# Optimization experiments

Measured on AMD Instinct MI355X. Metric: run time of the kernel, lower is better.

The kernel has to match this reference:

```python
import jax, jax.numpy as jnp
import numpy as np

B, C, H, W = 8, 3, 512, 512
EPS = 2e-4
N_ITER = 10  # n_iter_max default in TvChambolleDenoiser.forward


def setup_inputs() -> dict:
    key = jax.random.key(0)
    k1, k2 = jax.random.split(key)
    image = jax.random.normal(k1, (B, C, H, W), dtype=jnp.float32)
    # per-image denoising strength, typical TV weights
    weight = jax.random.uniform(k2, (B,), dtype=jnp.float32, minval=0.05, maxval=0.15)
    return {"image": image, "weight": weight}


def _denoise_tv_2d(img, w, eps=EPS, n_iter=N_ITER):
    """Chambolle TV denoising of a single 2D image (faithful to the torch loop)."""
    tau = 0.25  # 1 / (2 * ndim), ndim = 2
    numel = img.shape[0] * img.shape[1]

    def body(carry, i):
        pt, out, E_init, E_prev, done = carry
        # divergence of dual variable pt: dt = -pt.sum(0); dt[1:,:] += pt[0,:-1,:]; dt[:,1:] += pt[1,:,:-1]
        dt = -(pt[0] + pt[1])
        dt = dt.at[1:, :].add(pt[0, :-1, :])
        dt = dt.at[:, 1:].add(pt[1, :, :-1])
        out_new = jnp.where(i > 0, img + dt, img)
        Et = jnp.where(i > 0, jnp.sum(dt * dt), jnp.float32(0.0))
        # forward finite differences, zero-padded at the far boundary (gt stays 0 there)
        g0 = jnp.pad(out_new[1:, :] - out_new[:-1, :], ((0, 1), (0, 0)))
        g1 = jnp.pad(out_new[:, 1:] - out_new[:, :-1], ((0, 0), (0, 1)))
        s = g0 * g0 + g1 * g1
        # safe sqrt (forward value identical; avoids NaN grads at exact zeros)
        norm = jnp.sqrt(jnp.where(s > 0, s, 1.0)) * (s > 0)
        Et = (Et + w * jnp.sum(norm)) / numel
        gt = jnp.stack([g0, g1])  # [2, H, W]
        pt_new = (pt - tau * gt) / (1.0 + (tau / w) * norm)[None]
        E_init_new = jnp.where(i == 0, Et, E_init)
        converged = (i > 0) & (jnp.abs(E_prev - Et) < eps * E_init_new)
        # once converged (break in the torch loop), freeze all state
        pt = jnp.where(done, pt, pt_new)
        out = jnp.where(done, out, out_new)
        E_prev = jnp.where(done, E_prev, Et)
        E_init = jnp.where(done, E_init, E_init_new)
        done = done | converged
        return (pt, out, E_init, E_prev, done), None

    carry0 = (
        jnp.zeros((2,) + img.shape, img.dtype),  # pt
        img,                                      # out
        jnp.float32(0.0),                         # E_init
        jnp.float32(0.0),                         # E_previous
        jnp.bool_(False),                         # done
    )
    (pt, out, E_init, E_prev, done), _ = jax.lax.scan(body, carry0, jnp.arange(n_iter))
    return out


def reference(image, weight):
    b, c, h, w = image.shape
    imgs = image.reshape(b * c, h, w)          # each (batch, channel) slice denoised independently
    ws = jnp.repeat(weight, c)                 # per-batch weight shared across channels
    out = jax.vmap(_denoise_tv_2d)(imgs, ws)
    return out.reshape(b, c, h, w)
```

## Files before the change

### kernel.cpp

```cpp
#include <hip/hip_runtime.h>
#include <hip/hip_fp16.h>
#include <math.h>
#include <stdint.h>

#define HH 512
#define WW 512
#define NIMG 24
#define CCH 3
#define TAU 0.25f
#define TVEPS 2e-4f
#define NUMEL 262144.0f

#define LSF 69
#define LSH 70


__device__ __forceinline__ float2 h2f(uint32_t v) {
    __half2 h; *reinterpret_cast<uint32_t*>(&h) = v;
    return __half22float2(h);
}
__device__ __forceinline__ uint32_t f2h2(float a, float b) {
    __half2 h = __floats2half2_rn(a, b);
    return *reinterpret_cast<uint32_t*>(&h);
}
__device__ __forceinline__ void h4_to_f(uint2 hv, float* f) {
    float2 a = h2f(hv.x), b = h2f(hv.y);
    f[0] = a.x; f[1] = a.y; f[2] = b.x; f[3] = b.y;
}

struct Smem {
    uint32_t PT[68 * LSF];
    float    OA[68 * LSF];
    __half   IM[68 * LSH];
};

__device__ __forceinline__ int SUMIX(int slot, int arr, int im) {
    return ((slot * 4 + arr) * NIMG + im) * 64;
}

__device__ void stage_pt_im(Smem& S, const uint32_t* __restrict__ ptg,
                            const __half* __restrict__ hI,
                            int x0, int y0, int tid) {
    for (int idx = tid; idx < 68 * 34; idx += 256) {
        int r = idx / 34, mq = idx - r * 34;
        int c = 2 * mq;
        int y = y0 - 2 + r, x = x0 - 2 + c;
        uint2 pv = make_uint2(0u, 0u);
        uint32_t iv = 0u;
        if ((unsigned)y < (unsigned)HH && (unsigned)x < (unsigned)WW) {
            size_t off = (size_t)y * WW + x;
            pv = *(const uint2*)(ptg + off);
            iv = *(const uint32_t*)(hI + off);
        }
        S.PT[r * LSF + c] = pv.x;
        S.PT[r * LSF + c + 1] = pv.y;
        *(uint32_t*)&S.IM[r * LSH + c] = iv;
    }
}

template <bool ACC>
__device__ float phase_outA(Smem& S, int tid) {
    float acc = 0.f;
    for (int idx = tid; idx < 67 * 67; idx += 256) {
        int r = idx / 67, c = idx - r * 67;
        r += 1; c += 1;
        float2 cf = h2f(S.PT[r * LSF + c]);
        float up = h2f(S.PT[(r - 1) * LSF + c]).x;
        float lf = h2f(S.PT[r * LSF + c - 1]).y;
        float im = __half2float(S.IM[r * LSH + c]);
        float oa = im + (-(cf.x + cf.y) + up + lf);
        S.OA[r * LSF + c] = oa;
        if (ACC) {
            if (r >= 2 && r < 66 && c >= 2 && c < 66) {
                float d = oa - im;
                acc += d * d;
            }
        }
    }
    return acc;
}

template <bool ACC>
__device__ float phase_ptA(Smem& S, int x0, int y0, int tid, float tw) {
    float acc = 0.f;
    for (int idx = tid; idx < 66 * 66; idx += 256) {
        int r = idx / 66, c = idx - r * 66;
        r += 1; c += 1;
        int y = y0 - 2 + r, x = x0 - 2 + c;
        if ((unsigned)y < (unsigned)HH && (unsigned)x < (unsigned)WW) {
            float o = S.OA[r * LSF + c];
            float g0 = (y < HH - 1) ? S.OA[(r + 1) * LSF + c] - o : 0.f;
            float g1 = (x < WW - 1) ? S.OA[r * LSF + c + 1] - o : 0.f;
            float ss2 = g0 * g0 + g1 * g1;
            float nrm = (ss2 > 0.f) ? sqrtf(ss2) : 0.f;
            if (ACC) {
                if (r >= 2 && r < 66 && c >= 2 && c < 66) acc += nrm;
            }
            float inv = __builtin_amdgcn_rcpf(1.f + tw * nrm);
            float2 cf = h2f(S.PT[r * LSF + c]);
            S.PT[r * LSF + c] = f2h2((cf.x - TAU * g0) * inv, (cf.y - TAU * g1) * inv);
        } else {
            S.PT[r * LSF + c] = 0u;
        }
    }
    return acc;
}

template <bool ACC>
__device__ float phase_outB(Smem& S, int tid) {
    float acc = 0.f;
    for (int idx = tid; idx < 65 * 65; idx += 256) {
        int r = idx / 65, c = idx - r * 65;
        r += 2; c += 2;
        float2 cf = h2f(S.PT[r * LSF + c]);
        float im = __half2float(S.IM[r * LSH + c]);
        float ob = im + (-(cf.x + cf.y) + h2f(S.PT[(r - 1) * LSF + c]).x
                         + h2f(S.PT[r * LSF + c - 1]).y);
        S.OA[r * LSF + c] = ob;
        if (ACC) {
            if (r < 66 && c < 66) {
                float d = ob - im;
                acc += d * d;
            }
        }
    }
    return acc;
}

__device__ float phase_ptB_store(Smem& S, uint32_t* __restrict__ poutI,
                                 int x0, int y0, int tid, float tw) {
    const int tx = tid & 15, ry = tid >> 4;
    const int gxb = x0 + 4 * tx;
    float acc = 0.f;
    #pragma unroll
    for (int i = 0; i < 4; ++i) {
        int gy = y0 + ry + 16 * i;
        int r = 2 + ry + 16 * i;
        uint32_t pv[4];
        #pragma unroll
        for (int j = 0; j < 4; ++j) {
            int c = 2 + 4 * tx + j;
            float o = S.OA[r * LSF + c];
            float g0 = (gy < HH - 1) ? S.OA[(r + 1) * LSF + c] - o : 0.f;
            float g1 = (gxb + j < WW - 1) ? S.OA[r * LSF + c + 1] - o : 0.f;
            float ss2 = g0 * g0 + g1 * g1;
            float nrm = (ss2 > 0.f) ? sqrtf(ss2) : 0.f;
            acc += nrm;
            float inv = __builtin_amdgcn_rcpf(1.f + tw * nrm);
            float2 cf = h2f(S.PT[r * LSF + c]);
            pv[j] = f2h2((cf.x - TAU * g0) * inv, (cf.y - TAU * g1) * inv);
        }
        *(uint4*)(poutI + (size_t)gy * WW + gxb) = make_uint4(pv[0], pv[1], pv[2], pv[3]);
    }
    return acc;
}

__device__ __forceinline__ void red4_store(float a, float b, float c, float d,
                                           float* pa, float* pb, float* pc, float* pdd,
                                           int tid) {
    for (int off = 32; off > 0; off >>= 1) {
        a += __shfl_down(a, off, 64);
        b += __shfl_down(b, off, 64);
        c += __shfl_down(c, off, 64);
        d += __shfl_down(d, off, 64);
    }
    __shared__ float sr[4][4];
    int wave = tid >> 6, lane = tid & 63;
    if (lane == 0) { sr[0][wave] = a; sr[1][wave] = b; sr[2][wave] = c; sr[3][wave] = d; }
    __syncthreads();
    if (tid == 0) {
        *pa = (sr[0][0] + sr[0][1]) + (sr[0][2] + sr[0][3]);
        *pb = (sr[1][0] + sr[1][1]) + (sr[1][2] + sr[1][3]);
        *pc = (sr[2][0] + sr[2][1]) + (sr[2][2] + sr[2][3]);
        *pdd = (sr[3][0] + sr[3][1]) + (sr[3][2] + sr[3][3]);
    }
}

__global__ __launch_bounds__(256, 4) void tv_step0(
    const float* __restrict__ img, const float* __restrict__ weight,
    __half* __restrict__ imgh, uint32_t* __restrict__ ptout,
    float* __restrict__ pn0)
{
    const int im = blockIdx.z;
    const int bid = blockIdx.y * 8 + blockIdx.x;
    const float w = weight[im / CCH];
    const int x0 = blockIdx.x * 64, y0 = blockIdx.y * 64;
    const float* imgI = img + (size_t)im * HH * WW;
    __half* hI = imgh + (size_t)im * HH * WW;
    uint32_t* pI = ptout + (size_t)im * HH * WW;
    __shared__ float s[65][68];
    const int tid = threadIdx.x;
    const int tx = tid & 15, ry = tid >> 4;
    const int gx = x0 + 4 * tx;

    float o[4][4];
    #pragma unroll
    for (int i = 0; i < 4; ++i) {
        int ey = ry + 16 * i, gy = y0 + ey;
        float4 v = *(const float4*)(imgI + (size_t)gy * WW + gx);
        o[i][0] = v.x; o[i][1] = v.y; o[i][2] = v.z; o[i][3] = v.w;
        *(float4*)&s[ey][4 * tx] = v;
    }
    if (tx == 15 && x0 + 64 < WW) {
        #pragma unroll
        for (int i = 0; i < 4; ++i) {
            int ey = ry + 16 * i, gy = y0 + ey;
            s[ey][64] = imgI[(size_t)gy * WW + x0 + 64];
        }
    }
    if (ry == 0 && y0 + 64 < HH) {
        *(float4*)&s[64][4 * tx] = *(const float4*)(imgI + (size_t)(y0 + 64) * WW + gx);
    }
    __syncthreads();

    float accn = 0.f;
    const float tw = TAU / w;
    #pragma unroll
    for (int i = 0; i < 4; ++i) {
        int ey = ry + 16 * i, gy = y0 + ey;
        float4 dn = *(float4*)&s[ey + 1][4 * tx];
        float rt_sh = __shfl_down(o[i][0], 1, 64);
        float rt = (tx == 15) ? s[ey][64] : rt_sh;
        float dnv[4] = {dn.x, dn.y, dn.z, dn.w};
        uint32_t pv[4];
        #pragma unroll
        for (int j = 0; j < 4; ++j) {
            float ov = o[i][j];
            float g0 = (gy < HH - 1) ? dnv[j] - ov : 0.f;
            float rn = (j < 3) ? o[i][j + 1] : rt;
            float g1 = (gx + j < WW - 1) ? rn - ov : 0.f;
            float ss2 = g0 * g0 + g1 * g1;
            float nrm = (ss2 > 0.f) ? sqrtf(ss2) : 0.f;
            accn += nrm;
            float inv = __builtin_amdgcn_rcpf(1.f + tw * nrm);
            pv[j] = f2h2(-TAU * g0 * inv, -TAU * g1 * inv);
        }
        size_t off = (size_t)gy * WW + gx;
        *(uint4*)(pI + off) = make_uint4(pv[0], pv[1], pv[2], pv[3]);
        *(uint2*)(hI + off) = make_uint2(f2h2(o[i][0], o[i][1]), f2h2(o[i][2], o[i][3]));
    }
    for (int off = 32; off > 0; off >>= 1) accn += __shfl_down(accn, off, 64);
    __shared__ float sr[4];
    if ((tid & 63) == 0) sr[tid >> 6] = accn;
    __syncthreads();
    if (tid == 0) pn0[im * 64 + bid] = (sr[0] + sr[1]) + (sr[2] + sr[3]);
}

__global__ __launch_bounds__(256, 3) void tv_fused(
    int m,
    const __half* __restrict__ imgh, const float* __restrict__ weight,
    const uint32_t* __restrict__ pt_in, uint32_t* __restrict__ pt_out,
    float* __restrict__ sc, float* __restrict__ sums)
{
    const int im = blockIdx.z;
    const int bid = blockIdx.y * 8 + blockIdx.x;
    const int tid = threadIdx.x;
    const float w = weight[im / CCH];

    __shared__ int sh_done;
    {
        const int sIn = (m - 1) & 1;
        if (tid < 64) {
            float da = 0.f, na = 0.f, db = 0.f, nb = 0.f;
            if (m == 1) {
                na = sums[SUMIX(0, 1, im) + tid];
            } else {
                da = sums[SUMIX(sIn, 0, im) + tid];
                na = sums[SUMIX(sIn, 1, im) + tid];
                db = sums[SUMIX(sIn, 2, im) + tid];
                nb = sums[SUMIX(sIn, 3, im) + tid];
            }
            for (int off = 32; off > 0; off >>= 1) {
                da += __shfl_down(da, off, 64);
                na += __shfl_down(na, off, 64);
                db += __shfl_down(db, off, 64);
                nb += __shfl_down(nb, off, 64);
            }
            if (tid == 0) {
                float Eprev, Einit; int done, lastk;
                if (m == 1) {
                    float E0 = w * na / NUMEL;
                    Eprev = E0; Einit = E0; done = 0; lastk = 0;
                } else {
                    const float* sI = sc + sIn * 128;
                    Eprev = sI[im]; Einit = sI[32 + im];
                    done = ((const int*)sI)[64 + im];
                    lastk = ((const int*)sI)[96 + im];
                    if (!done) {
                        float Et = (da + w * na) / NUMEL;
                        if (fabsf(Eprev - Et) < TVEPS * Einit) { done = 1; lastk = 2 * m - 3; }
                        else {
                            Eprev = Et;
                            Et = (db + w * nb) / NUMEL;
                            if (fabsf(Eprev - Et) < TVEPS * Einit) { done = 1; lastk = 2 * m - 2; }
                            else Eprev = Et;
                        }
                    }
                }
                if (bid == 0) {
                    float* sO = sc + (m & 1) * 128;
                    sO[im] = Eprev; sO[32 + im] = Einit;
                    ((int*)sO)[64 + im] = done;
                    ((int*)sO)[96 + im] = lastk;
                }
                sh_done = done;
            }
        }
    }
    __syncthreads();
    if (sh_done) return;

    const int x0 = blockIdx.x * 64, y0 = blockIdx.y * 64;
    const float tw = TAU / w;
    const uint32_t* pinI = pt_in + (size_t)im * HH * WW;
    uint32_t* poutI = pt_out + (size_t)im * HH * WW;
    const __half* hI = imgh + (size_t)im * HH * WW;

    __shared__ Smem S;
    stage_pt_im(S, pinI, hI, x0, y0, tid);
    __syncthreads();
    float a_d = phase_outA<true>(S, tid);
    __syncthreads();
    float a_n = phase_ptA<true>(S, x0, y0, tid, tw);
    __syncthreads();
    float b_d = phase_outB<true>(S, tid);
    __syncthreads();
    float b_n = phase_ptB_store(S, poutI, x0, y0, tid, tw);

    const int sOut = m & 1;
    red4_store(a_d, a_n, b_d, b_n,
               &sums[SUMIX(sOut, 0, im) + bid], &sums[SUMIX(sOut, 1, im) + bid],
               &sums[SUMIX(sOut, 2, im) + bid], &sums[SUMIX(sOut, 3, im) + bid], tid);
}

__global__ __launch_bounds__(256, 3) void tv_out(
    const float* __restrict__ img, float* __restrict__ out,
    const uint32_t* __restrict__ ptA, const uint32_t* __restrict__ ptB,
    const __half* __restrict__ imgh, const float* __restrict__ weight,
    const float* __restrict__ sc, const float* __restrict__ sums)
{
    const int im = blockIdx.z;
    const int tid = threadIdx.x;
    const float w = weight[im / CCH];

    __shared__ int2 shk;
    {
        const float* sI = sc;
        int done = ((const int*)sI)[64 + im];
        int lastk = ((const int*)sI)[96 + im];
        if (!done && tid < 64) {
            float da = sums[SUMIX(0, 0, im) + tid];
            float na = sums[SUMIX(0, 1, im) + tid];
            float db = sums[SUMIX(0, 2, im) + tid];
            float nb = sums[SUMIX(0, 3, im) + tid];
            for (int off = 32; off > 0; off >>= 1) {
                da += __shfl_down(da, off, 64);
                na += __shfl_down(na, off, 64);
                db += __shfl_down(db, off, 64);
                nb += __shfl_down(nb, off, 64);
            }
            if (tid == 0) {
                float Eprev = sI[im], Einit = sI[32 + im];
                float Et = (da + w * na) / NUMEL;
                if (fabsf(Eprev - Et) < TVEPS * Einit) { done = 1; lastk = 7; }
                else {
                    Eprev = Et;
                    Et = (db + w * nb) / NUMEL;
                    if (fabsf(Eprev - Et) < TVEPS * Einit) { done = 1; lastk = 8; }
                }
            }
        }
        if (tid == 0) { shk.x = done; shk.y = lastk; }
    }
    __syncthreads();
    const int k = shk.x ? shk.y : 9;

    const float* imgI = img + (size_t)im * HH * WW;
    float* outI = out + (size_t)im * HH * WW;
    const int x0 = blockIdx.x * 64, y0 = blockIdx.y * 64;
    const int tx = tid & 15, ry = tid >> 4;
    const int gx = x0 + 4 * tx;

    if (k & 1) {
        const uint32_t* p = ((((k - 1) >> 1) & 1) ? ptB : ptA) + (size_t)im * HH * WW;
        #pragma unroll
        for (int i = 0; i < 4; ++i) {
            int gy = y0 + ry + 16 * i;
            size_t off = (size_t)gy * WW + gx;
            uint4 cv = *(const uint4*)(p + off);
            uint4 uv = make_uint4(0u, 0u, 0u, 0u);
            if (gy > 0) uv = *(const uint4*)(p + off - WW);
            uint32_t lf = (gx > 0) ? p[off - 1] : 0u;
            float4 iv = *(const float4*)(imgI + off);
            uint32_t cc[4] = {cv.x, cv.y, cv.z, cv.w};
            uint32_t uu[4] = {uv.x, uv.y, uv.z, uv.w};
            uint32_t lt[4] = {lf, cv.x, cv.y, cv.z};
            float ivv[4] = {iv.x, iv.y, iv.z, iv.w};
            float r[4];
            #pragma unroll
            for (int j = 0; j < 4; ++j) {
                float2 cf = h2f(cc[j]);
                r[j] = ivv[j] + (-(cf.x + cf.y) + h2f(uu[j]).x + h2f(lt[j]).y);
            }
            *(float4*)(outI + off) = make_float4(r[0], r[1], r[2], r[3]);
        }
    } else {
        const uint32_t* p = ((((k - 2) >> 1) & 1) ? ptB : ptA) + (size_t)im * HH * WW;
        const __half* hI = imgh + (size_t)im * HH * WW;
        const float tw = TAU / w;
        __shared__ Smem S;
        stage_pt_im(S, p, hI, x0, y0, tid);
        __syncthreads();
        phase_outA<false>(S, tid);
        __syncthreads();
        phase_ptA<false>(S, x0, y0, tid, tw);
        __syncthreads();
        #pragma unroll
        for (int i = 0; i < 4; ++i) {
            int gy = y0 + ry + 16 * i;
            int r = 2 + ry + 16 * i;
            size_t off = (size_t)gy * WW + gx;
            float4 iv = *(const float4*)(imgI + off);
            float ivv[4] = {iv.x, iv.y, iv.z, iv.w};
            float rr[4];
            #pragma unroll
            for (int j = 0; j < 4; ++j) {
                int c = 2 + 4 * tx + j;
                float2 cf = h2f(S.PT[r * LSF + c]);
                float up = h2f(S.PT[(r - 1) * LSF + c]).x;
                float lf = h2f(S.PT[r * LSF + c - 1]).y;
                rr[j] = ivv[j] + (-(cf.x + cf.y) + up + lf);
            }
            *(float4*)(outI + off) = make_float4(rr[0], rr[1], rr[2], rr[3]);
        }
    }
}

extern "C" void kernel_launch(void* const* d_in, const int* in_sizes, int n_in,
                              void* d_out, int out_size, void* d_ws, size_t ws_size,
                              hipStream_t stream)
{
    const float* img = (const float*)d_in[0];
    const float* weight = (const float*)d_in[1];
    float* out = (float*)d_out;
    float* sc = (float*)d_ws;
    float* sums = (float*)((char*)d_ws + 4096);
    __half* imgh = (__half*)((char*)d_ws + 65536);
    uint32_t* ptA = (uint32_t*)((char*)d_ws + 12648448);
    uint32_t* ptB = (uint32_t*)((char*)d_ws + 37814272);

    dim3 grid(8, 8, NIMG);
    dim3 block(256);

    tv_step0<<<grid, block, 0, stream>>>(img, weight, imgh, ptA,
                                         sums + (0 * 4 + 1) * NIMG * 64);

    for (int m = 1; m <= 4; ++m) {
        uint32_t* pin  = (m & 1) ? ptA : ptB;
        uint32_t* pout = (m & 1) ? ptB : ptA;
        tv_fused<<<grid, block, 0, stream>>>(m, imgh, weight, pin, pout, sc, sums);
    }

    tv_out<<<grid, block, 0, stream>>>(img, out, ptA, ptB, imgh, weight, sc, sums);
}
```

Measured before the change: 280.2 us.

## Rewrite fused two-step kernel with register-resident overlapped tiles and LDS edge exchange

The fused two-iteration kernel now has each thread hold a 4x4 patch in registers over a 64x64 window that owns a 60x60 output tile, giving a 9x9 grid of overlapping blocks. Neighbour values travel through wave shuffles and a small LDS row-exchange buffer instead of the full padded shared-memory staging arrays. This cuts LDS traffic and the per-phase index arithmetic, and drops the large shared struct, which should allow more occupancy. In exchange it recomputes halo cells (more blocks, redundant loads) and widens the per-image partial-sum arrays to 81 entries, which are reduced across two waves.

```diff
diff --git a/kernel.cpp b/kernel.cpp
--- a/kernel.cpp
+++ b/kernel.cpp
@@ -11,6 +11,9 @@
 #define TVEPS 2e-4f
 #define NUMEL 262144.0f
 
+#define TSO 60
+#define NT 9
+
 #define LSF 69
 #define LSH 70
 
@@ -26,6 +29,31 @@
 __device__ __forceinline__ void h4_to_f(uint2 hv, float* f) {
     float2 a = h2f(hv.x), b = h2f(hv.y);
     f[0] = a.x; f[1] = a.y; f[2] = b.x; f[3] = b.y;
+}
+
+__device__ __forceinline__ int SUMIX(int slot, int arr, int im) {
+    return ((slot * 4 + arr) * NIMG + im) * 96;
+}
+
+__device__ __forceinline__ void red4_store(float a, float b, float c, float d,
+                                           float* pa, float* pb, float* pc, float* pdd,
+                                           int tid) {
+    for (int off = 32; off > 0; off >>= 1) {
+        a += __shfl_down(a, off, 64);
+        b += __shfl_down(b, off, 64);
+        c += __shfl_down(c, off, 64);
+        d += __shfl_down(d, off, 64);
+    }
+    __shared__ float sr[4][4];
+    int wave = tid >> 6, lane = tid & 63;
+    if (lane == 0) { sr[0][wave] = a; sr[1][wave] = b; sr[2][wave] = c; sr[3][wave] = d; }
+    __syncthreads();
+    if (tid == 0) {
+        *pa = (sr[0][0] + sr[0][1]) + (sr[0][2] + sr[0][3]);
+        *pb = (sr[1][0] + sr[1][1]) + (sr[1][2] + sr[1][3]);
+        *pc = (sr[2][0] + sr[2][1]) + (sr[2][2] + sr[2][3]);
+        *pdd = (sr[3][0] + sr[3][1]) + (sr[3][2] + sr[3][3]);
+    }
 }
 
 struct Smem {
@@ -33,10 +61,6 @@
     float    OA[68 * LSF];
     __half   IM[68 * LSH];
 };
-
-__device__ __forceinline__ int SUMIX(int slot, int arr, int im) {
-    return ((slot * 4 + arr) * NIMG + im) * 64;
-}
 
 __device__ void stage_pt_im(Smem& S, const uint32_t* __restrict__ ptg,
                             const __half* __restrict__ hI,
@@ -58,9 +82,7 @@
     }
 }
 
-template <bool ACC>
-__device__ float phase_outA(Smem& S, int tid) {
-    float acc = 0.f;
+__device__ void phase_outA_x(Smem& S, int tid) {
     for (int idx = tid; idx < 67 * 67; idx += 256) {
         int r = idx / 67, c = idx - r * 67;
         r += 1; c += 1;
@@ -68,21 +90,11 @@
         float up = h2f(S.PT[(r - 1) * LSF + c]).x;
         float lf = h2f(S.PT[r * LSF + c - 1]).y;
         float im = __half2float(S.IM[r * LSH + c]);
-        float oa = im + (-(cf.x + cf.y) + up + lf);
-        S.OA[r * LSF + c] = oa;
-        if (ACC) {
-            if (r >= 2 && r < 66 && c >= 2 && c < 66) {
-                float d = oa - im;
-                acc += d * d;
-            }
-        }
-    }
-    return acc;
-}
-
-template <bool ACC>
-__device__ float phase_ptA(Smem& S, int x0, int y0, int tid, float tw) {
-    float acc = 0.f;
+        S.OA[r * LSF + c] = im + (-(cf.x + cf.y) + up + lf);
+    }
+}
+
+__device__ void phase_ptA_x(Smem& S, int x0, int y0, int tid, float tw) {
     for (int idx = tid; idx < 66 * 66; idx += 256) {
         int r = idx / 66, c = idx - r * 66;
         r += 1; c += 1;
@@ -93,86 +105,12 @@
             float g1 = (x < WW - 1) ? S.OA[r * LSF + c + 1] - o : 0.f;
             float ss2 = g0 * g0 + g1 * g1;
             float nrm = (ss2 > 0.f) ? sqrtf(ss2) : 0.f;
-            if (ACC) {
-                if (r >= 2 && r < 66 && c >= 2 && c < 66) acc += nrm;
-            }
             float inv = __builtin_amdgcn_rcpf(1.f + tw * nrm);
             float2 cf = h2f(S.PT[r * LSF + c]);
             S.PT[r * LSF + c] = f2h2((cf.x - TAU * g0) * inv, (cf.y - TAU * g1) * inv);
         } else {
             S.PT[r * LSF + c] = 0u;
         }
-    }
-    return acc;
-}
-
-template <bool ACC>
-__device__ float phase_outB(Smem& S, int tid) {
-    float acc = 0.f;
-    for (int idx = tid; idx < 65 * 65; idx += 256) {
-        int r = idx / 65, c = idx - r * 65;
-        r += 2; c += 2;
-        float2 cf = h2f(S.PT[r * LSF + c]);
-        float im = __half2float(S.IM[r * LSH + c]);
-        float ob = im + (-(cf.x + cf.y) + h2f(S.PT[(r - 1) * LSF + c]).x
-                         + h2f(S.PT[r * LSF + c - 1]).y);
-        S.OA[r * LSF + c] = ob;
-        if (ACC) {
-            if (r < 66 && c < 66) {
-                float d = ob - im;
-                acc += d * d;
-            }
-        }
-    }
-    return acc;
-}
-
-__device__ float phase_ptB_store(Smem& S, uint32_t* __restrict__ poutI,
-                                 int x0, int y0, int tid, float tw) {
-    const int tx = tid & 15, ry = tid >> 4;
-    const int gxb = x0 + 4 * tx;
-    float acc = 0.f;
-    #pragma unroll
-    for (int i = 0; i < 4; ++i) {
-        int gy = y0 + ry + 16 * i;
-        int r = 2 + ry + 16 * i;
-        uint32_t pv[4];
-        #pragma unroll
-        for (int j = 0; j < 4; ++j) {
-            int c = 2 + 4 * tx + j;
-            float o = S.OA[r * LSF + c];
-            float g0 = (gy < HH - 1) ? S.OA[(r + 1) * LSF + c] - o : 0.f;
-            float g1 = (gxb + j < WW - 1) ? S.OA[r * LSF + c + 1] - o : 0.f;
-            float ss2 = g0 * g0 + g1 * g1;
-            float nrm = (ss2 > 0.f) ? sqrtf(ss2) : 0.f;
-            acc += nrm;
-            float inv = __builtin_amdgcn_rcpf(1.f + tw * nrm);
-            float2 cf = h2f(S.PT[r * LSF + c]);
-            pv[j] = f2h2((cf.x - TAU * g0) * inv, (cf.y - TAU * g1) * inv);
-        }
-        *(uint4*)(poutI + (size_t)gy * WW + gxb) = make_uint4(pv[0], pv[1], pv[2], pv[3]);
-    }
-    return acc;
-}
-
-__device__ __forceinline__ void red4_store(float a, float b, float c, float d,
-                                           float* pa, float* pb, float* pc, float* pdd,
-                                           int tid) {
-    for (int off = 32; off > 0; off >>= 1) {
-        a += __shfl_down(a, off, 64);
-        b += __shfl_down(b, off, 64);
-        c += __shfl_down(c, off, 64);
-        d += __shfl_down(d, off, 64);
-    }
-    __shared__ float sr[4][4];
-    int wave = tid >> 6, lane = tid & 63;
-    if (lane == 0) { sr[0][wave] = a; sr[1][wave] = b; sr[2][wave] = c; sr[3][wave] = d; }
-    __syncthreads();
-    if (tid == 0) {
-        *pa = (sr[0][0] + sr[0][1]) + (sr[0][2] + sr[0][3]);
-        *pb = (sr[1][0] + sr[1][1]) + (sr[1][2] + sr[1][3]);
-        *pc = (sr[2][0] + sr[2][1]) + (sr[2][2] + sr[2][3]);
-        *pdd = (sr[3][0] + sr[3][1]) + (sr[3][2] + sr[3][3]);
     }
 }
 
@@ -243,7 +181,7 @@
     __shared__ float sr[4];
     if ((tid & 63) == 0) sr[tid >> 6] = accn;
     __syncthreads();
-    if (tid == 0) pn0[im * 64 + bid] = (sr[0] + sr[1]) + (sr[2] + sr[3]);
+    if (tid == 0) pn0[im * 96 + bid] = (sr[0] + sr[1]) + (sr[2] + sr[3]);
 }
 
 __global__ __launch_bounds__(256, 3) void tv_fused(
@@ -253,82 +191,247 @@
     float* __restrict__ sc, float* __restrict__ sums)
 {
     const int im = blockIdx.z;
-    const int bid = blockIdx.y * 8 + blockIdx.x;
+    const int bx = blockIdx.x, by = blockIdx.y;
+    const int bid = by * NT + bx;
     const int tid = threadIdx.x;
     const float w = weight[im / CCH];
 
     __shared__ int sh_done;
+    __shared__ float hsum[2][4];
     {
         const int sIn = (m - 1) & 1;
-        if (tid < 64) {
-            float da = 0.f, na = 0.f, db = 0.f, nb = 0.f;
-            if (m == 1) {
-                na = sums[SUMIX(0, 1, im) + tid];
-            } else {
-                da = sums[SUMIX(sIn, 0, im) + tid];
-                na = sums[SUMIX(sIn, 1, im) + tid];
-                db = sums[SUMIX(sIn, 2, im) + tid];
-                nb = sums[SUMIX(sIn, 3, im) + tid];
-            }
+        float da = 0.f, na = 0.f, db = 0.f, nb = 0.f;
+        if (m == 1) {
+            if (tid < 64) na = sums[SUMIX(0, 1, im) + tid];
+        } else if (tid < 81) {
+            da = sums[SUMIX(sIn, 0, im) + tid];
+            na = sums[SUMIX(sIn, 1, im) + tid];
+            db = sums[SUMIX(sIn, 2, im) + tid];
+            nb = sums[SUMIX(sIn, 3, im) + tid];
+        }
+        if (tid < 128) {
             for (int off = 32; off > 0; off >>= 1) {
                 da += __shfl_down(da, off, 64);
                 na += __shfl_down(na, off, 64);
                 db += __shfl_down(db, off, 64);
                 nb += __shfl_down(nb, off, 64);
             }
-            if (tid == 0) {
-                float Eprev, Einit; int done, lastk;
-                if (m == 1) {
-                    float E0 = w * na / NUMEL;
-                    Eprev = E0; Einit = E0; done = 0; lastk = 0;
-                } else {
-                    const float* sI = sc + sIn * 128;
-                    Eprev = sI[im]; Einit = sI[32 + im];
-                    done = ((const int*)sI)[64 + im];
-                    lastk = ((const int*)sI)[96 + im];
-                    if (!done) {
-                        float Et = (da + w * na) / NUMEL;
-                        if (fabsf(Eprev - Et) < TVEPS * Einit) { done = 1; lastk = 2 * m - 3; }
-                        else {
-                            Eprev = Et;
-                            Et = (db + w * nb) / NUMEL;
-                            if (fabsf(Eprev - Et) < TVEPS * Einit) { done = 1; lastk = 2 * m - 2; }
-                            else Eprev = Et;
-                        }
+            if ((tid & 63) == 0) {
+                hsum[tid >> 6][0] = da; hsum[tid >> 6][1] = na;
+                hsum[tid >> 6][2] = db; hsum[tid >> 6][3] = nb;
+            }
+        }
+        __syncthreads();
+        if (tid == 0) {
+            float tda = hsum[0][0] + hsum[1][0];
+            float tna = hsum[0][1] + hsum[1][1];
+            float tdb = hsum[0][2] + hsum[1][2];
+            float tnb = hsum[0][3] + hsum[1][3];
+            float Eprev, Einit; int done, lastk;
+            if (m == 1) {
+                float E0 = w * tna / NUMEL;
+                Eprev = E0; Einit = E0; done = 0; lastk = 0;
+            } else {
+                const float* sI = sc + ((m - 1) & 1) * 128;
+                Eprev = sI[im]; Einit = sI[32 + im];
+                done = ((const int*)sI)[64 + im];
+                lastk = ((const int*)sI)[96 + im];
+                if (!done) {
+                    float Et = (tda + w * tna) / NUMEL;
+                    if (fabsf(Eprev - Et) < TVEPS * Einit) { done = 1; lastk = 2 * m - 3; }
+                    else {
+                        Eprev = Et;
+                        Et = (tdb + w * tnb) / NUMEL;
+                        if (fabsf(Eprev - Et) < TVEPS * Einit) { done = 1; lastk = 2 * m - 2; }
+                        else Eprev = Et;
                     }
                 }
-                if (bid == 0) {
-                    float* sO = sc + (m & 1) * 128;
-                    sO[im] = Eprev; sO[32 + im] = Einit;
-                    ((int*)sO)[64 + im] = done;
-                    ((int*)sO)[96 + im] = lastk;
-                }
-                sh_done = done;
-            }
+            }
+            if (bid == 0) {
+                float* sO = sc + (m & 1) * 128;
+                sO[im] = Eprev; sO[32 + im] = Einit;
+                ((int*)sO)[64 + im] = done;
+                ((int*)sO)[96 + im] = lastk;
+            }
+            sh_done = done;
         }
     }
     __syncthreads();
     if (sh_done) return;
 
-    const int x0 = blockIdx.x * 64, y0 = blockIdx.y * 64;
     const float tw = TAU / w;
     const uint32_t* pinI = pt_in + (size_t)im * HH * WW;
     uint32_t* poutI = pt_out + (size_t)im * HH * WW;
     const __half* hI = imgh + (size_t)im * HH * WW;
 
-    __shared__ Smem S;
-    stage_pt_im(S, pinI, hI, x0, y0, tid);
-    __syncthreads();
-    float a_d = phase_outA<true>(S, tid);
-    __syncthreads();
-    float a_n = phase_ptA<true>(S, x0, y0, tid, tw);
-    __syncthreads();
-    float b_d = phase_outB<true>(S, tid);
-    __syncthreads();
-    float b_n = phase_ptB_store(S, poutI, x0, y0, tid, tw);
+    const int tx = tid & 15, ty = tid >> 4;
+    const int wx0 = TSO * bx - 2, wy0 = TSO * by - 2;
+    const int cx0 = wx0 + 4 * tx;
+    const int ry0 = wy0 + 4 * ty;
+
+    __shared__ uint4  XP[16][16];
+    __shared__ float4 XO[16][16];
+
+    uint32_t c[4][4];
+    uint32_t ihp[4][2];
+    const bool interior = (wx0 >= 0) && (wx0 + 64 <= WW) && (wy0 >= 0) && (wy0 + 64 <= HH);
+    if (interior) {
+        #pragma unroll
+        for (int i = 0; i < 4; ++i) {
+            size_t off = (size_t)(ry0 + i) * WW + cx0;
+            uint2 a = *(const uint2*)(pinI + off);
+            uint2 b = *(const uint2*)(pinI + off + 2);
+            c[i][0] = a.x; c[i][1] = a.y; c[i][2] = b.x; c[i][3] = b.y;
+            ihp[i][0] = *(const uint32_t*)(hI + off);
+            ihp[i][1] = *(const uint32_t*)(hI + off + 2);
+        }
+    } else {
+        #pragma unroll
+        for (int i = 0; i < 4; ++i) {
+            int gy = ry0 + i;
+            unsigned short us[4];
+            #pragma unroll
+            for (int j = 0; j < 4; ++j) {
+                int gxj = cx0 + j;
+                bool in = ((unsigned)gy < (unsigned)HH) && ((unsigned)gxj < (unsigned)WW);
+                c[i][j] = in ? pinI[(size_t)gy * WW + gxj] : 0u;
+                us[j] = in ? *(const unsigned short*)(hI + (size_t)gy * WW + gxj)
+                           : (unsigned short)0;
+            }
+            ihp[i][0] = (uint32_t)us[0] | ((uint32_t)us[1] << 16);
+            ihp[i][1] = (uint32_t)us[2] | ((uint32_t)us[3] << 16);
+        }
+    }
+    XP[ty][tx] = make_uint4(c[3][0], c[3][1], c[3][2], c[3][3]);
+    __syncthreads();
+
+    float o[4][4];
+    float accda = 0.f;
+    {
+        uint4 up4 = (ty > 0) ? XP[ty - 1][tx] : make_uint4(0u, 0u, 0u, 0u);
+        uint32_t ua[4] = {up4.x, up4.y, up4.z, up4.w};
+        #pragma unroll
+        for (int i = 0; i < 4; ++i) {
+            uint32_t lw = __shfl_up(c[i][3], 1, 64);
+            int gy = ry0 + i;
+            bool r_ok = (unsigned)(4 * ty + i - 2) < 60u && gy < HH;
+            #pragma unroll
+            for (int j = 0; j < 4; ++j) {
+                float2 cf = h2f(c[i][j]);
+                float up = (i > 0) ? h2f(c[i - 1][j]).x : h2f(ua[j]).x;
+                float le = (j > 0) ? h2f(c[i][j - 1]).y : h2f(lw).y;
+                float dv = -(cf.x + cf.y) + up + le;
+                float2 i2 = h2f(ihp[i][j >> 1]);
+                float imv = (j & 1) ? i2.y : i2.x;
+                o[i][j] = imv + dv;
+                bool own = r_ok && ((unsigned)(4 * tx + j - 2) < 60u) && (cx0 + j < WW);
+                accda += own ? dv * dv : 0.f;
+            }
+        }
+    }
+
+    uint32_t pa[4][4];
+    float accna = 0.f;
+    XO[ty][tx] = make_float4(o[0][0], o[0][1], o[0][2], o[0][3]);
+    __syncthreads();
+    {
+        float4 b4 = (ty < 15) ? XO[ty + 1][tx] : make_float4(0.f, 0.f, 0.f, 0.f);
+        float bel[4] = {b4.x, b4.y, b4.z, b4.w};
+        #pragma unroll
+        for (int i = 0; i < 4; ++i) {
+            float rsh = __shfl_down(o[i][0], 1, 64);
+            int gy = ry0 + i;
+            bool r_ok = (unsigned)(4 * ty + i - 2) < 60u && gy < HH;
+            #pragma unroll
+            for (int j = 0; j < 4; ++j) {
+                int gxj = cx0 + j;
+                float ov = o[i][j];
+                float below = (i < 3) ? o[i + 1][j] : bel[j];
+                float right = (j < 3) ? o[i][j + 1] : rsh;
+                float g0 = (gy < HH - 1) ? below - ov : 0.f;
+                float g1 = (gxj < WW - 1) ? right - ov : 0.f;
+                float ss2 = g0 * g0 + g1 * g1;
+                float nrm = (ss2 > 0.f) ? sqrtf(ss2) : 0.f;
+                float inv = __builtin_amdgcn_rcpf(1.f + tw * nrm);
+                float2 cf = h2f(c[i][j]);
+                uint32_t pvv = f2h2((cf.x - TAU * g0) * inv, (cf.y - TAU * g1) * inv);
+                bool vp = ((unsigned)gy < (unsigned)HH) && ((unsigned)gxj < (unsigned)WW);
+                pa[i][j] = vp ? pvv : 0u;
+                bool own = r_ok && ((unsigned)(4 * tx + j - 2) < 60u) && (gxj < WW);
+                accna += own ? nrm : 0.f;
+            }
+        }
+    }
+
+    float ob[4][4];
+    float accdb = 0.f;
+    XP[ty][tx] = make_uint4(pa[3][0], pa[3][1], pa[3][2], pa[3][3]);
+    __syncthreads();
+    {
+        uint4 up4 = (ty > 0) ? XP[ty - 1][tx] : make_uint4(0u, 0u, 0u, 0u);
+        uint32_t ua[4] = {up4.x, up4.y, up4.z, up4.w};
+        #pragma unroll
+        for (int i = 0; i < 4; ++i) {
+            uint32_t lw = __shfl_up(pa[i][3], 1, 64);
+            int gy = ry0 + i;
+            bool r_ok = (unsigned)(4 * ty + i - 2) < 60u && gy < HH;
+            #pragma unroll
+            for (int j = 0; j < 4; ++j) {
+                float2 cf = h2f(pa[i][j]);
+                float up = (i > 0) ? h2f(pa[i - 1][j]).x : h2f(ua[j]).x;
+                float le = (j > 0) ? h2f(pa[i][j - 1]).y : h2f(lw).y;
+                float dv = -(cf.x + cf.y) + up + le;
+                float2 i2 = h2f(ihp[i][j >> 1]);
+                float imv = (j & 1) ? i2.y : i2.x;
+                ob[i][j] = imv + dv;
+                bool own = r_ok && ((unsigned)(4 * tx + j - 2) < 60u) && (cx0 + j < WW);
+                accdb += own ? dv * dv : 0.f;
+            }
+        }
+    }
+
+    float accnb = 0.f;
+    XO[ty][tx] = make_float4(ob[0][0], ob[0][1], ob[0][2], ob[0][3]);
+    __syncthreads();
+    {
+        float4 b4 = (ty < 15) ? XO[ty + 1][tx] : make_float4(0.f, 0.f, 0.f, 0.f);
+        float bel[4] = {b4.x, b4.y, b4.z, b4.w};
+        #pragma unroll
+        for (int i = 0; i < 4; ++i) {
+            float rsh = __shfl_down(ob[i][0], 1, 64);
+            int gy = ry0 + i;
+            bool r_ok = ((unsigned)(4 * ty + i - 2) < 60u) && (gy < HH);
+            uint32_t pv[4];
+            #pragma unroll
+            for (int j = 0; j < 4; ++j) {
+                int gxj = cx0 + j;
+                float ov = ob[i][j];
+                float below = (i < 3) ? ob[i + 1][j] : bel[j];
+                float right = (j < 3) ? ob[i][j + 1] : rsh;
+                float g0 = (gy < HH - 1) ? below - ov : 0.f;
+                float g1 = (gxj < WW - 1) ? right - ov : 0.f;
+                float ss2 = g0 * g0 + g1 * g1;
+                float nrm = (ss2 > 0.f) ? sqrtf(ss2) : 0.f;
+                float inv = __builtin_amdgcn_rcpf(1.f + tw * nrm);
+                float2 cf = h2f(pa[i][j]);
+                uint32_t pvv = f2h2((cf.x - TAU * g0) * inv, (cf.y - TAU * g1) * inv);
+                bool vp = ((unsigned)gy < (unsigned)HH) && ((unsigned)gxj < (unsigned)WW);
+                pv[j] = vp ? pvv : 0u;
+                bool own = r_ok && ((unsigned)(4 * tx + j - 2) < 60u) && (gxj < WW);
+                accnb += own ? nrm : 0.f;
+            }
+            if (r_ok) {
+                size_t off = (size_t)gy * WW + cx0;
+                if (tx > 0 && cx0 < WW)
+                    *(uint2*)(poutI + off) = make_uint2(pv[0], pv[1]);
+                if (tx < 15 && cx0 + 2 < WW)
+                    *(uint2*)(poutI + off + 2) = make_uint2(pv[2], pv[3]);
+            }
+        }
+    }
 
     const int sOut = m & 1;
-    red4_store(a_d, a_n, b_d, b_n,
+    red4_store(accda, accna, accdb, accnb,
                &sums[SUMIX(sOut, 0, im) + bid], &sums[SUMIX(sOut, 1, im) + bid],
                &sums[SUMIX(sOut, 2, im) + bid], &sums[SUMIX(sOut, 3, im) + bid], tid);
 }
@@ -344,33 +447,48 @@
     const float w = weight[im / CCH];
 
     __shared__ int2 shk;
+    __shared__ float hsum[2][4];
     {
         const float* sI = sc;
         int done = ((const int*)sI)[64 + im];
         int lastk = ((const int*)sI)[96 + im];
-        if (!done && tid < 64) {
-            float da = sums[SUMIX(0, 0, im) + tid];
-            float na = sums[SUMIX(0, 1, im) + tid];
-            float db = sums[SUMIX(0, 2, im) + tid];
-            float nb = sums[SUMIX(0, 3, im) + tid];
+        float da = 0.f, na = 0.f, db = 0.f, nb = 0.f;
+        if (!done && tid < 81) {
+            da = sums[SUMIX(0, 0, im) + tid];
+            na = sums[SUMIX(0, 1, im) + tid];
+            db = sums[SUMIX(0, 2, im) + tid];
+            nb = sums[SUMIX(0, 3, im) + tid];
+        }
+        if (tid < 128) {
             for (int off = 32; off > 0; off >>= 1) {
                 da += __shfl_down(da, off, 64);
                 na += __shfl_down(na, off, 64);
                 db += __shfl_down(db, off, 64);
                 nb += __shfl_down(nb, off, 64);
             }
-            if (tid == 0) {
+            if ((tid & 63) == 0) {
+                hsum[tid >> 6][0] = da; hsum[tid >> 6][1] = na;
+                hsum[tid >> 6][2] = db; hsum[tid >> 6][3] = nb;
+            }
+        }
+        __syncthreads();
+        if (tid == 0) {
+            if (!done) {
+                float tda = hsum[0][0] + hsum[1][0];
+                float tna = hsum[0][1] + hsum[1][1];
+                float tdb = hsum[0][2] + hsum[1][2];
+                float tnb = hsum[0][3] + hsum[1][3];
                 float Eprev = sI[im], Einit = sI[32 + im];
-                float Et = (da + w * na) / NUMEL;
+                float Et = (tda + w * tna) / NUMEL;
                 if (fabsf(Eprev - Et) < TVEPS * Einit) { done = 1; lastk = 7; }
                 else {
                     Eprev = Et;
-                    Et = (db + w * nb) / NUMEL;
+                    Et = (tdb + w * tnb) / NUMEL;
                     if (fabsf(Eprev - Et) < TVEPS * Einit) { done = 1; lastk = 8; }
                 }
             }
-        }
-        if (tid == 0) { shk.x = done; shk.y = lastk; }
+            shk.x = done; shk.y = lastk;
+        }
     }
     __syncthreads();
     const int k = shk.x ? shk.y : 9;
@@ -411,9 +529,9 @@
         __shared__ Smem S;
         stage_pt_im(S, p, hI, x0, y0, tid);
         __syncthreads();
-        phase_outA<false>(S, tid);
+        phase_outA_x(S, tid);
         __syncthreads();
-        phase_ptA<false>(S, x0, y0, tid, tw);
+        phase_ptA_x(S, x0, y0, tid, tw);
         __syncthreads();
         #pragma unroll
         for (int i = 0; i < 4; ++i) {
@@ -425,10 +543,10 @@
             float rr[4];
             #pragma unroll
             for (int j = 0; j < 4; ++j) {
-                int c = 2 + 4 * tx + j;
-                float2 cf = h2f(S.PT[r * LSF + c]);
-                float up = h2f(S.PT[(r - 1) * LSF + c]).x;
-                float lf = h2f(S.PT[r * LSF + c - 1]).y;
+                int cix = 2 + 4 * tx + j;
+                float2 cf = h2f(S.PT[r * LSF + cix]);
+                float up = h2f(S.PT[(r - 1) * LSF + cix]).x;
+                float lf = h2f(S.PT[r * LSF + cix - 1]).y;
                 rr[j] = ivv[j] + (-(cf.x + cf.y) + up + lf);
             }
             *(float4*)(outI + off) = make_float4(rr[0], rr[1], rr[2], rr[3]);
@@ -445,21 +563,20 @@
     float* out = (float*)d_out;
     float* sc = (float*)d_ws;
     float* sums = (float*)((char*)d_ws + 4096);
-    __half* imgh = (__half*)((char*)d_ws + 65536);
-    uint32_t* ptA = (uint32_t*)((char*)d_ws + 12648448);
-    uint32_t* ptB = (uint32_t*)((char*)d_ws + 37814272);
-
-    dim3 grid(8, 8, NIMG);
+    __half* imgh = (__half*)((char*)d_ws + 131072);
+    uint32_t* ptA = (uint32_t*)((char*)d_ws + 12713984);
+    uint32_t* ptB = (uint32_t*)((char*)d_ws + 37879808);
+
     dim3 block(256);
 
-    tv_step0<<<grid, block, 0, stream>>>(img, weight, imgh, ptA,
-                                         sums + (0 * 4 + 1) * NIMG * 64);
+    float* pn0 = sums + 1 * NIMG * 96;
+    tv_step0<<<dim3(8, 8, NIMG), block, 0, stream>>>(img, weight, imgh, ptA, pn0);
 
     for (int m = 1; m <= 4; ++m) {
         uint32_t* pin  = (m & 1) ? ptA : ptB;
         uint32_t* pout = (m & 1) ? ptB : ptA;
-        tv_fused<<<grid, block, 0, stream>>>(m, imgh, weight, pin, pout, sc, sums);
-    }
-
-    tv_out<<<grid, block, 0, stream>>>(img, out, ptA, ptB, imgh, weight, sc, sums);
-}
+        tv_fused<<<dim3(NT, NT, NIMG), block, 0, stream>>>(m, imgh, weight, pin, pout, sc, sums);
+    }
+
+    tv_out<<<dim3(8, 8, NIMG), block, 0, stream>>>(img, out, ptA, ptB, imgh, weight, sc, sums);
+}
```

Measured after the change: 231.8 us. -17.3%, faster.
